# Optimization experiments

Measured on AMD Instinct MI355X. Metric: run time of the kernel, lower is better.

The kernel has to match this reference:

```python
import jax, jax.numpy as jnp
import numpy as np

B, S, D_IN = 4, 256, 1024
ATTN, HD = 1024, 64
H = ATTN // HD  # 16
C = 4096          # n_classes
R, CR, SC = 256, 1024, 2048  # n_roots, n_classroots, n_subclasses
FF = int(ATTN * 3.0)  # 3072
EPS = 1e-5


def setup_inputs() -> dict:
    key = jax.random.key(0)
    ks = jax.random.split(key, 16)
    x = jax.random.normal(ks[0], (B, S, D_IN), dtype=jnp.float32)
    cls = jax.random.normal(ks[1], (H, C, HD), dtype=jnp.float32)
    roots = jax.random.normal(ks[2], (H, R, HD), dtype=jnp.float32)
    # IndexedAdd indices: row 0 selects from src, row 1 scatters into dst
    clsroots_idx = jnp.stack([
        jax.random.randint(ks[3], (CR,), 0, R, dtype=jnp.int32),
        jax.random.randint(ks[4], (CR,), 0, C, dtype=jnp.int32)])
    clscls_idx = jnp.stack([
        jax.random.randint(ks[5], (SC,), 0, C, dtype=jnp.int32),
        jax.random.randint(ks[6], (SC,), 0, C, dtype=jnp.int32)])
    clsroots_w = jax.random.uniform(ks[7], (H, CR, 1), dtype=jnp.float32, minval=0.5, maxval=1.5)
    clscls_w = jax.random.uniform(ks[8], (H, SC, 1), dtype=jnp.float32, minval=0.5, maxval=1.5)
    sc = 1.0 / np.sqrt(D_IN)
    kv_w = jax.random.uniform(ks[9], (2 * ATTN, D_IN), dtype=jnp.float32, minval=-sc, maxval=sc)
    ln_gamma = jnp.ones((ATTN,), dtype=jnp.float32)
    ln_beta = jnp.zeros((ATTN,), dtype=jnp.float32)
    sa = 1.0 / np.sqrt(ATTN)
    ff_in_w = jax.random.uniform(ks[10], (2 * FF, ATTN), dtype=jnp.float32, minval=-sa, maxval=sa)
    sf = 1.0 / np.sqrt(FF)
    ff_out_w = jax.random.uniform(ks[11], (ATTN, FF), dtype=jnp.float32, minval=-sf, maxval=sf)
    out_w = jax.random.uniform(ks[12], (C, ATTN, 2), dtype=jnp.float32, minval=-sa, maxval=sa)
    return {"x": x, "cls": cls, "roots": roots, "clsroots_w": clsroots_w,
            "clscls_w": clscls_w, "kv_w": kv_w, "ln_gamma": ln_gamma, "ln_beta": ln_beta,
            "ff_in_w": ff_in_w, "ff_out_w": ff_out_w, "out_w": out_w,
            "clsroots_idx": clsroots_idx, "clscls_idx": clscls_idx}


def _rmsnorm(t):
    return t * jax.lax.rsqrt(jnp.mean(t * t, axis=-1, keepdims=True) + EPS)


def _silu(t):
    return t * jax.nn.sigmoid(t)


def reference(x, cls, roots, clsroots_w, clscls_w, kv_w, ln_gamma, ln_beta,
              ff_in_w, ff_out_w, out_w, clsroots_idx, clscls_idx):
    # --- hierarchical query build (IndexedAdd chain) ---
    qr = _rmsnorm(roots)                                        # [H,R,E]
    q = cls.at[:, clsroots_idx[1], :].add(qr[:, clsroots_idx[0], :] * clsroots_w)
    q_det = jax.lax.stop_gradient(q)                            # clscls uses q.detach()
    q = q.at[:, clscls_idx[1], :].add(q_det[:, clscls_idx[0], :] * clscls_w)
    q = _rmsnorm(q)                                             # [H,C,E]
    # --- KV projection + QK-RMSNorm cross-attention ---
    kv = (x @ kv_w.T).reshape(B, S, 2, H, HD)                   # '(n h e)' split
    k = jnp.transpose(kv[:, :, 0], (0, 2, 1, 3))                # [B,H,S,E]
    v = jnp.transpose(kv[:, :, 1], (0, 2, 1, 3))                # [B,H,S,E]
    k = _rmsnorm(k)
    scores = jnp.einsum('hce,bhse->bhcs', q, k) / np.sqrt(HD)   # [B,H,C,S]
    attn = jax.nn.softmax(scores, axis=-1)
    o = jnp.einsum('bhcs,bhse->bhce', attn, v)                  # [B,H,C,E]
    o = jnp.transpose(o, (0, 2, 1, 3)).reshape(B, C, ATTN)      # [B,C,ATTN]
    # --- SwiGLU FFN with pre-LayerNorm + residual ---
    mu = jnp.mean(o, axis=-1, keepdims=True)
    var = jnp.mean((o - mu) ** 2, axis=-1, keepdims=True)
    f = (o - mu) * jax.lax.rsqrt(var + EPS) * ln_gamma + ln_beta
    f = f @ ff_in_w.T                                           # [B,C,2*FF]
    f1, f2 = f[..., :FF], f[..., FF:]
    h = (_silu(f1) * f2) @ ff_out_w.T
    z = o + h                                                   # [B,C,ATTN]
    # --- per-class BatchLinear + SwiGLU output ---
    y = jnp.einsum('bca,cao->bco', z, out_w)                    # [B,C,2]
    out = _silu(y[..., 0:1]) * y[..., 1:2]                      # [B,C,1]
    return out
```

## Files before the change

kernel.cpp:

```cpp
#include <hip/hip_runtime.h>
#include <math.h>

#define EPS 1e-5f

typedef __bf16 bf16x8 __attribute__((ext_vector_type(8)));
typedef __bf16 bf16x4 __attribute__((ext_vector_type(4)));
typedef float f32x4 __attribute__((ext_vector_type(4)));

#define GPTR(p) ((const __attribute__((address_space(1))) void*)(p))
#define LPTR(p) ((__attribute__((address_space(3))) void*)(p))

__device__ __forceinline__ float wave_sum(float v) {
#pragma unroll
    for (int o = 32; o; o >>= 1) v += __shfl_xor(v, o);
    return v;
}

__global__ __launch_bounds__(256) void scatter1(const float* __restrict__ roots,
                                                const float* __restrict__ w,
                                                const int* __restrict__ idx,
                                                float* __restrict__ q) {
    int unit = (blockIdx.x << 2) + (threadIdx.x >> 6);
    int lane = threadIdx.x & 63;
    int h = unit >> 10;
    int i = unit & 1023;
    int r = idx[i];
    int c = idx[1024 + i];
    float val = roots[(h * 256 + r) * 64 + lane];
    float ss = wave_sum(val * val);
    float rs = rsqrtf(ss * (1.f / 64.f) + EPS);
    atomicAdd(&q[(h * 4096 + c) * 64 + lane], val * rs * w[(h << 10) + i]);
}

__global__ __launch_bounds__(256) void scatter2(const float* __restrict__ qdet,
                                                const float* __restrict__ w,
                                                const int* __restrict__ idx,
                                                float* __restrict__ q) {
    int unit = (blockIdx.x << 2) + (threadIdx.x >> 6);
    int lane = threadIdx.x & 63;
    int h = unit >> 11;
    int i = unit & 2047;
    int c1 = idx[i];
    int c2 = idx[2048 + i];
    float val = qdet[(h * 4096 + c1) * 64 + lane] * w[(h << 11) + i];
    atomicAdd(&q[(h * 4096 + c2) * 64 + lane], val);
}

__global__ __launch_bounds__(256) void rms_q_bf(const float* __restrict__ q,
                                                __bf16* __restrict__ qb) {
    int unit = (blockIdx.x << 2) + (threadIdx.x >> 6);
    int lane = threadIdx.x & 63;
    float v = q[(size_t)unit * 64 + lane];
    float ss = wave_sum(v * v);
    float r = v * rsqrtf(ss * (1.f / 64.f) + EPS);
    qb[(size_t)unit * 64 + lane] = (__bf16)r;
}

__global__ __launch_bounds__(256) void split8(const float* __restrict__ in,
                                              __bf16* __restrict__ hi,
                                              __bf16* __restrict__ lo, int n8) {
    int i = blockIdx.x * 256 + threadIdx.x;
    if (i >= n8) return;
    const float4* p = (const float4*)in + (size_t)i * 2;
    float4 u0 = p[0], u1 = p[1];
    float f[8] = {u0.x, u0.y, u0.z, u0.w, u1.x, u1.y, u1.z, u1.w};
    bf16x8 vh, vl;
#pragma unroll
    for (int j = 0; j < 8; ++j) {
        vh[j] = (__bf16)f[j];
        vl[j] = (__bf16)(f[j] - (float)vh[j]);
    }
    *((bf16x8*)hi + i) = vh;
    *((bf16x8*)lo + i) = vl;
}

__global__ __launch_bounds__(256) void gemm_kv_mfma(const __bf16* __restrict__ Ah,
                                                    const __bf16* __restrict__ Al,
                                                    const __bf16* __restrict__ Bh,
                                                    const __bf16* __restrict__ Bl,
                                                    float* __restrict__ Cout) {
    __shared__ __bf16 sAh[64 * 64], sAl[64 * 64];
    __shared__ __bf16 sBh[128 * 64], sBl[128 * 64];
    int tid = threadIdx.x;
    int bn = blockIdx.x, bm = blockIdx.y;
    int lane = tid & 63;
    int w = tid >> 6;
    int wr = (w >> 1) * 32, wc = (w & 1) * 64;
    int frow = lane & 15, fk = (lane >> 4) * 8;
    f32x4 acc[2][4] = {};
    const __bf16* Ahb = Ah + (size_t)(bm * 64) * 1024;
    const __bf16* Alb = Al + (size_t)(bm * 64) * 1024;
    const __bf16* Bhb = Bh + (size_t)(bn * 128) * 1024;
    const __bf16* Blb = Bl + (size_t)(bn * 128) * 1024;
    for (int k0 = 0; k0 < 1024; k0 += 64) {
#pragma unroll
        for (int t = 0; t < 2; ++t) {
            int e = (t * 256 + tid) * 8;
            int r = e >> 6, c = e & 63;
            __builtin_amdgcn_global_load_lds(GPTR(Ahb + (size_t)r * 1024 + k0 + c), LPTR(sAh + e), 16, 0, 0);
            __builtin_amdgcn_global_load_lds(GPTR(Alb + (size_t)r * 1024 + k0 + c), LPTR(sAl + e), 16, 0, 0);
        }
#pragma unroll
        for (int t = 0; t < 4; ++t) {
            int e = (t * 256 + tid) * 8;
            int r = e >> 6, c = e & 63;
            __builtin_amdgcn_global_load_lds(GPTR(Bhb + (size_t)r * 1024 + k0 + c), LPTR(sBh + e), 16, 0, 0);
            __builtin_amdgcn_global_load_lds(GPTR(Blb + (size_t)r * 1024 + k0 + c), LPTR(sBl + e), 16, 0, 0);
        }
        __syncthreads();
#pragma unroll
        for (int ks = 0; ks < 2; ++ks) {
            bf16x8 ah[2], al[2], bh2[4], bl2[4];
#pragma unroll
            for (int m = 0; m < 2; ++m) {
                ah[m] = *(const bf16x8*)(sAh + (wr + m * 16 + frow) * 64 + ks * 32 + fk);
                al[m] = *(const bf16x8*)(sAl + (wr + m * 16 + frow) * 64 + ks * 32 + fk);
            }
#pragma unroll
            for (int n = 0; n < 4; ++n) {
                bh2[n] = *(const bf16x8*)(sBh + (wc + n * 16 + frow) * 64 + ks * 32 + fk);
                bl2[n] = *(const bf16x8*)(sBl + (wc + n * 16 + frow) * 64 + ks * 32 + fk);
            }
#pragma unroll
            for (int m = 0; m < 2; ++m)
#pragma unroll
                for (int n = 0; n < 4; ++n) {
                    acc[m][n] = __builtin_amdgcn_mfma_f32_16x16x32_bf16(ah[m], bh2[n], acc[m][n], 0, 0, 0);
                    acc[m][n] = __builtin_amdgcn_mfma_f32_16x16x32_bf16(ah[m], bl2[n], acc[m][n], 0, 0, 0);
                    acc[m][n] = __builtin_amdgcn_mfma_f32_16x16x32_bf16(al[m], bh2[n], acc[m][n], 0, 0, 0);
                }
        }
        __syncthreads();
    }
    int crow = (lane >> 4) * 4, ccol = lane & 15;
#pragma unroll
    for (int m = 0; m < 2; ++m)
#pragma unroll
        for (int n = 0; n < 4; ++n)
#pragma unroll
            for (int j = 0; j < 4; ++j) {
                int row = bm * 64 + wr + m * 16 + crow + j;
                int col = bn * 128 + wc + n * 16 + ccol;
                Cout[(size_t)row * 2048 + col] = acc[m][n][j];
            }
}

__global__ __launch_bounds__(256) void kvsplit_bf(const float* __restrict__ kv,
                                                  __bf16* __restrict__ kb) {
    int unit = (blockIdx.x << 2) + (threadIdx.x >> 6);
    int lane = threadIdx.x & 63;
    int b = unit >> 12;
    int h = (unit >> 8) & 15;
    int s = unit & 255;
    float kvl = kv[(size_t)(b * 256 + s) * 2048 + (h << 6) + lane];
    float ss = wave_sum(kvl * kvl);
    float kn = kvl * rsqrtf(ss * (1.f / 64.f) + EPS);
    kb[(size_t)unit * 64 + lane] = (__bf16)kn;
}

__global__ __launch_bounds__(256) void vtrans_bf(const float* __restrict__ kv,
                                                 __bf16* __restrict__ vt) {
    __shared__ float T[64][65];
    int bh = blockIdx.x >> 2;
    int sc = blockIdx.x & 3;
    int b = bh >> 4, h = bh & 15;
    int tid = threadIdx.x;
    int s0 = sc * 64;
    int sl = tid >> 2, d0 = (tid & 3) * 16;
    const float* src = kv + (size_t)(b * 256 + s0 + sl) * 2048 + 1024 + (h << 6) + d0;
#pragma unroll
    for (int t = 0; t < 4; ++t) {
        float4 v4 = *(const float4*)(src + t * 4);
        T[sl][d0 + t * 4 + 0] = v4.x;
        T[sl][d0 + t * 4 + 1] = v4.y;
        T[sl][d0 + t * 4 + 2] = v4.z;
        T[sl][d0 + t * 4 + 3] = v4.w;
    }
    __syncthreads();
    int dr = tid >> 2, c0 = (tid & 3) * 16;
    bf16x8 h0, h1;
#pragma unroll
    for (int jj = 0; jj < 8; ++jj) h0[jj] = (__bf16)T[c0 + jj][dr];
#pragma unroll
    for (int jj = 0; jj < 8; ++jj) h1[jj] = (__bf16)T[c0 + 8 + jj][dr];
    size_t base = (size_t)bh * 16384 + (size_t)dr * 256 + s0 + c0;
    *(bf16x8*)(vt + base) = h0;
    *(bf16x8*)(vt + base + 8) = h1;
}

__global__ __launch_bounds__(256) void attn_mfma(const __bf16* __restrict__ qb,
                                                 const __bf16* __restrict__ kb,
                                                 const __bf16* __restrict__ vtb,
                                                 __bf16* __restrict__ ob) {
    __shared__ __bf16 P[64 * 264];
    __shared__ float wred[8][64];
    __shared__ float denomL[64];
    __shared__ __bf16 Ot[64 * 72];

    int wg = blockIdx.x;
    int swz = (wg & 7) * 512 + (wg >> 3);
    int bh = swz >> 6;
    int qt = swz & 63;
    int b = bh >> 4, h = bh & 15;
    int tid = threadIdx.x;
    int lane = tid & 63;
    int w = tid >> 6;
    int frow = lane & 15;
    int fk = (lane >> 4) * 8;
    int crow = (lane >> 4) * 4;
    int ccol = lane & 15;
    int q0 = qt * 64;
    int wsr = w * 64;

    const __bf16* kh = kb + (size_t)bh * 16384;
    const __bf16* qh = qb + (size_t)h * 262144 + (size_t)q0 * 64;

    f32x4 acc[4][4] = {};
#pragma unroll
    for (int ks = 0; ks < 2; ++ks) {
        bf16x8 kf[4];
#pragma unroll
        for (int m = 0; m < 4; ++m)
            kf[m] = *(const bf16x8*)(kh + (wsr + m * 16 + frow) * 64 + ks * 32 + fk);
#pragma unroll
        for (int n = 0; n < 4; ++n) {
            bf16x8 qf = *(const bf16x8*)(qh + (n * 16 + frow) * 64 + ks * 32 + fk);
#pragma unroll
            for (int m = 0; m < 4; ++m)
                acc[m][n] = __builtin_amdgcn_mfma_f32_16x16x32_bf16(kf[m], qf, acc[m][n], 0, 0, 0);
        }
    }
#pragma unroll
    for (int m = 0; m < 4; ++m)
#pragma unroll
        for (int n = 0; n < 4; ++n)
#pragma unroll
            for (int j = 0; j < 4; ++j) acc[m][n][j] *= 0.125f;

    float lm[4];
#pragma unroll
    for (int n = 0; n < 4; ++n) {
        float v = -1e30f;
#pragma unroll
        for (int m = 0; m < 4; ++m)
#pragma unroll
            for (int j = 0; j < 4; ++j) v = fmaxf(v, acc[m][n][j]);
        v = fmaxf(v, __shfl_xor(v, 16));
        v = fmaxf(v, __shfl_xor(v, 32));
        lm[n] = v;
    }
    if (lane < 16) {
#pragma unroll
        for (int n = 0; n < 4; ++n) wred[w][n * 16 + lane] = lm[n];
    }
    __syncthreads();
    float gm[4];
#pragma unroll
    for (int n = 0; n < 4; ++n) {
        int qq = n * 16 + ccol;
        gm[n] = fmaxf(fmaxf(wred[0][qq], wred[1][qq]), fmaxf(wred[2][qq], wred[3][qq]));
    }
    float lsum[4] = {0.f, 0.f, 0.f, 0.f};
#pragma unroll
    for (int m = 0; m < 4; ++m)
#pragma unroll
        for (int n = 0; n < 4; ++n)
#pragma unroll
            for (int j = 0; j < 4; ++j) {
                float p = __expf(acc[m][n][j] - gm[n]);
                acc[m][n][j] = p;
                lsum[n] += p;
            }
#pragma unroll
    for (int n = 0; n < 4; ++n) {
        float v = lsum[n];
        v += __shfl_xor(v, 16);
        v += __shfl_xor(v, 32);
        lsum[n] = v;
    }
    if (lane < 16) {
#pragma unroll
        for (int n = 0; n < 4; ++n) wred[4 + w][n * 16 + lane] = lsum[n];
    }
#pragma unroll
    for (int m = 0; m < 4; ++m)
#pragma unroll
        for (int n = 0; n < 4; ++n) {
            bf16x4 pv;
#pragma unroll
            for (int j = 0; j < 4; ++j) pv[j] = (__bf16)acc[m][n][j];
            *(bf16x4*)(P + (n * 16 + ccol) * 264 + wsr + m * 16 + crow) = pv;
        }
    __syncthreads();
    if (tid < 64)
        denomL[tid] = wred[4][tid] + wred[5][tid] + wred[6][tid] + wred[7][tid];

    const __bf16* vh = vtb + (size_t)bh * 16384;
    f32x4 accO[4] = {};
#pragma unroll
    for (int ks = 0; ks < 8; ++ks) {
        bf16x8 pf = *(const bf16x8*)(P + (w * 16 + frow) * 264 + ks * 32 + fk);
#pragma unroll
        for (int m = 0; m < 4; ++m) {
            bf16x8 vf = *(const bf16x8*)(vh + (m * 16 + frow) * 256 + ks * 32 + fk);
            accO[m] = __builtin_amdgcn_mfma_f32_16x16x32_bf16(vf, pf, accO[m], 0, 0, 0);
        }
    }
    __syncthreads();
    float rd = 1.0f / denomL[w * 16 + ccol];
#pragma unroll
    for (int m = 0; m < 4; ++m) {
        bf16x4 ov;
#pragma unroll
        for (int j = 0; j < 4; ++j) ov[j] = (__bf16)(accO[m][j] * rd);
        *(bf16x4*)(Ot + (w * 16 + ccol) * 72 + m * 16 + crow) = ov;
    }
    __syncthreads();
    {
        int qq = tid >> 2, dc = tid & 3;
        bf16x8 o0 = *(const bf16x8*)(Ot + qq * 72 + dc * 16);
        bf16x8 o1 = *(const bf16x8*)(Ot + qq * 72 + dc * 16 + 8);
        size_t base = (size_t)((b << 12) + q0 + qq) * 1024 + (h << 6) + dc * 16;
        *(bf16x8*)(ob + base) = o0;
        *(bf16x8*)(ob + base + 8) = o1;
    }
}

__global__ __launch_bounds__(256) void cvt_bf16(const float* __restrict__ in,
                                                __bf16* __restrict__ out, int n8) {
    int i = blockIdx.x * 256 + threadIdx.x;
    if (i >= n8) return;
    const float4* p = (const float4*)in + (size_t)i * 2;
    float4 u0 = p[0], u1 = p[1];
    bf16x8 v;
    v[0] = (__bf16)u0.x; v[1] = (__bf16)u0.y; v[2] = (__bf16)u0.z; v[3] = (__bf16)u0.w;
    v[4] = (__bf16)u1.x; v[5] = (__bf16)u1.y; v[6] = (__bf16)u1.z; v[7] = (__bf16)u1.w;
    *((bf16x8*)out + i) = v;
}

__global__ __launch_bounds__(256) void ln_stats(const __bf16* __restrict__ ob,
                                                float* __restrict__ mu,
                                                float* __restrict__ rstd) {
    __shared__ float r0[4], r1[4];
    int row = blockIdx.x;
    int tid = threadIdx.x;
    const bf16x4* op = (const bf16x4*)(ob + (size_t)row * 1024);
    bf16x4 v = op[tid];
    float s = 0, sq = 0;
#pragma unroll
    for (int j = 0; j < 4; ++j) { float f = (float)v[j]; s += f; sq += f * f; }
    s = wave_sum(s);
    sq = wave_sum(sq);
    if ((tid & 63) == 0) { r0[tid >> 6] = s; r1[tid >> 6] = sq; }
    __syncthreads();
    if (tid == 0) {
        float S = r0[0] + r0[1] + r0[2] + r0[3];
        float Q = r1[0] + r1[1] + r1[2] + r1[3];
        float m = S * (1.f / 1024.f);
        float var = Q * (1.f / 1024.f) - m * m;
        mu[row] = m;
        rstd[row] = rsqrtf(var + EPS);
    }
}

__global__ __launch_bounds__(256) void ln_apply(const __bf16* __restrict__ ob,
                                                const float* __restrict__ mu,
                                                const float* __restrict__ rstd,
                                                const float* __restrict__ gamma,
                                                const float* __restrict__ beta,
                                                __bf16* __restrict__ f, int R0) {
    int i = blockIdx.x * 256 + threadIdx.x;
    int row = i >> 7;
    int c8 = (i & 127) * 8;
    int gr = R0 + row;
    float m = mu[gr], rs = rstd[gr];
    bf16x8 ov = *((const bf16x8*)(ob + (size_t)gr * 1024 + c8));
    bf16x8 r;
#pragma unroll
    for (int j = 0; j < 8; ++j) {
        float v = (float)ov[j];
        r[j] = (__bf16)((v - m) * rs * gamma[c8 + j] + beta[c8 + j]);
    }
    *((bf16x8*)(f + (size_t)row * 1024 + c8)) = r;
}

__global__ __launch_bounds__(256) void gemm1_mfma(const __bf16* __restrict__ A,
                                                  const __bf16* __restrict__ W,
                                                  __bf16* __restrict__ U) {
    __shared__ __bf16 sA[128 * 64];
    __shared__ __bf16 sB1[128 * 64];
    __shared__ __bf16 sB2[128 * 64];
    const int K = 1024;
    int tid = threadIdx.x;
    int bn = blockIdx.x, bm = blockIdx.y;
    int lane = tid & 63;
    int w = tid >> 6;
    int wr = (w >> 1) * 64, wc = (w & 1) * 64;
    f32x4 acc1[4][4] = {};
    f32x4 acc2[4][4] = {};
    const __bf16* Ab = A + (size_t)(bm * 128) * K;
    const __bf16* B1b = W + (size_t)(bn * 128) * K;
    const __bf16* B2b = W + (size_t)(3072 + bn * 128) * K;
    int frow = lane & 15, fk = (lane >> 4) * 8;
    for (int k0 = 0; k0 < K; k0 += 64) {
#pragma unroll
        for (int t = 0; t < 4; ++t) {
            int e = (t * 256 + tid) * 8;
            int r = e >> 6, c = e & 63;
            __builtin_amdgcn_global_load_lds(GPTR(Ab + (size_t)r * K + k0 + c), LPTR(sA + e), 16, 0, 0);
            __builtin_amdgcn_global_load_lds(GPTR(B1b + (size_t)r * K + k0 + c), LPTR(sB1 + e), 16, 0, 0);
            __builtin_amdgcn_global_load_lds(GPTR(B2b + (size_t)r * K + k0 + c), LPTR(sB2 + e), 16, 0, 0);
        }
        __syncthreads();
#pragma unroll
        for (int ks = 0; ks < 2; ++ks) {
            bf16x8 a[4], b1[4], b2[4];
#pragma unroll
            for (int m = 0; m < 4; ++m)
                a[m] = *(const bf16x8*)(sA + (wr + m * 16 + frow) * 64 + ks * 32 + fk);
#pragma unroll
            for (int n = 0; n < 4; ++n) {
                b1[n] = *(const bf16x8*)(sB1 + (wc + n * 16 + frow) * 64 + ks * 32 + fk);
                b2[n] = *(const bf16x8*)(sB2 + (wc + n * 16 + frow) * 64 + ks * 32 + fk);
            }
#pragma unroll
            for (int m = 0; m < 4; ++m)
#pragma unroll
                for (int n = 0; n < 4; ++n) {
                    acc1[m][n] = __builtin_amdgcn_mfma_f32_16x16x32_bf16(a[m], b1[n], acc1[m][n], 0, 0, 0);
                    acc2[m][n] = __builtin_amdgcn_mfma_f32_16x16x32_bf16(a[m], b2[n], acc2[m][n], 0, 0, 0);
                }
        }
        __syncthreads();
    }
    int crow = (lane >> 4) * 4, ccol = lane & 15;
#pragma unroll
    for (int m = 0; m < 4; ++m)
#pragma unroll
        for (int n = 0; n < 4; ++n)
#pragma unroll
            for (int j = 0; j < 4; ++j) {
                float f1 = acc1[m][n][j], f2 = acc2[m][n][j];
                float sg = f1 / (1.f + expf(-f1));
                int row = bm * 128 + wr + m * 16 + crow + j;
                int col = bn * 128 + wc + n * 16 + ccol;
                U[(size_t)row * 3072 + col] = (__bf16)(sg * f2);
            }
}

__global__ __launch_bounds__(256) void gemm2_mfma(const __bf16* __restrict__ U,
                                                  const __bf16* __restrict__ W2,
                                                  __bf16* __restrict__ Oz) {
    __shared__ __bf16 sA[128 * 64];
    __shared__ __bf16 sB[128 * 64];
    const int K = 3072;
    int tid = threadIdx.x;
    int bn = blockIdx.x, bm = blockIdx.y;
    int lane = tid & 63;
    int w = tid >> 6;
    int wr = (w >> 1) * 64, wc = (w & 1) * 64;
    f32x4 acc[4][4] = {};
    const __bf16* Ab = U + (size_t)(bm * 128) * K;
    const __bf16* Bb = W2 + (size_t)(bn * 128) * K;
    int frow = lane & 15, fk = (lane >> 4) * 8;
    for (int k0 = 0; k0 < K; k0 += 64) {
#pragma unroll
        for (int t = 0; t < 4; ++t) {
            int e = (t * 256 + tid) * 8;
            int r = e >> 6, c = e & 63;
            __builtin_amdgcn_global_load_lds(GPTR(Ab + (size_t)r * K + k0 + c), LPTR(sA + e), 16, 0, 0);
            __builtin_amdgcn_global_load_lds(GPTR(Bb + (size_t)r * K + k0 + c), LPTR(sB + e), 16, 0, 0);
        }
        __syncthreads();
#pragma unroll
        for (int ks = 0; ks < 2; ++ks) {
            bf16x8 a[4], b[4];
#pragma unroll
            for (int m = 0; m < 4; ++m)
                a[m] = *(const bf16x8*)(sA + (wr + m * 16 + frow) * 64 + ks * 32 + fk);
#pragma unroll
            for (int n = 0; n < 4; ++n)
                b[n] = *(const bf16x8*)(sB + (wc + n * 16 + frow) * 64 + ks * 32 + fk);
#pragma unroll
            for (int m = 0; m < 4; ++m)
#pragma unroll
                for (int n = 0; n < 4; ++n)
                    acc[m][n] = __builtin_amdgcn_mfma_f32_16x16x32_bf16(a[m], b[n], acc[m][n], 0, 0, 0);
        }
        __syncthreads();
    }
    int crow = (lane >> 4) * 4, ccol = lane & 15;
#pragma unroll
    for (int m = 0; m < 4; ++m)
#pragma unroll
        for (int n = 0; n < 4; ++n)
#pragma unroll
            for (int j = 0; j < 4; ++j) {
                int row = bm * 128 + wr + m * 16 + crow + j;
                int col = bn * 128 + wc + n * 16 + ccol;
                size_t off = (size_t)row * 1024 + col;
                float z = (float)Oz[off] + acc[m][n][j];
                Oz[off] = (__bf16)z;
            }
}

__global__ __launch_bounds__(256) void out_proj4(const __bf16* __restrict__ z,
                                                 const float* __restrict__ ow,
                                                 float* __restrict__ out) {
    __shared__ float red[4][8];
    int c = blockIdx.x;
    int tid = threadIdx.x;
    int a0 = tid * 4;
    const float4* w4 = (const float4*)(ow + (size_t)c * 2048);
    float4 wA = w4[tid * 2];
    float4 wB = w4[tid * 2 + 1];
    float y[8];
#pragma unroll
    for (int jj = 0; jj < 8; ++jj) y[jj] = 0.f;
#pragma unroll
    for (int bb = 0; bb < 4; ++bb) {
        bf16x4 zv = *(const bf16x4*)(z + (size_t)((bb << 12) + c) * 1024 + a0);
        float z0 = (float)zv[0], z1 = (float)zv[1], z2 = (float)zv[2], z3 = (float)zv[3];
        y[2 * bb] += z0 * wA.x + z1 * wA.z + z2 * wB.x + z3 * wB.z;
        y[2 * bb + 1] += z0 * wA.y + z1 * wA.w + z2 * wB.y + z3 * wB.w;
    }
#pragma unroll
    for (int jj = 0; jj < 8; ++jj) y[jj] = wave_sum(y[jj]);
    if ((tid & 63) == 0) {
#pragma unroll
        for (int jj = 0; jj < 8; ++jj) red[tid >> 6][jj] = y[jj];
    }
    __syncthreads();
    if (tid < 4) {
        float a0s = red[0][2 * tid] + red[1][2 * tid] + red[2][2 * tid] + red[3][2 * tid];
        float a1s = red[0][2 * tid + 1] + red[1][2 * tid + 1] + red[2][2 * tid + 1] + red[3][2 * tid + 1];
        out[(size_t)tid * 4096 + c] = a0s / (1.f + expf(-a0s)) * a1s;
    }
}

extern "C" void kernel_launch(void* const* d_in, const int* in_sizes, int n_in,
                              void* d_out, int out_size, void* d_ws, size_t ws_size,
                              hipStream_t stream) {
    const float* x = (const float*)d_in[0];
    const float* cls = (const float*)d_in[1];
    const float* roots = (const float*)d_in[2];
    const float* crw = (const float*)d_in[3];
    const float* ccw = (const float*)d_in[4];
    const float* kv_w = (const float*)d_in[5];
    const float* gamma = (const float*)d_in[6];
    const float* beta = (const float*)d_in[7];
    const float* ffin = (const float*)d_in[8];
    const float* ffout = (const float*)d_in[9];
    const float* ow = (const float*)d_in[10];
    const int* cridx = (const int*)d_in[11];
    const int* ccidx = (const int*)d_in[12];
    float* out = (float*)d_out;

    float* ws = (float*)d_ws;
    float* q = ws;
    float* kvb = ws + 4194304;
    __bf16* kbf = (__bf16*)(ws + 6291456);
    __bf16* vtb = (__bf16*)(ws + 6815744);
    __bf16* o_bf = (__bf16*)(ws + 8388608);
    __bf16* xhi = (__bf16*)(ws + 8388608);
    __bf16* xlo = (__bf16*)(ws + 8912896);
    __bf16* kvwhi = (__bf16*)(ws + 9437184);
    __bf16* kvwlo = (__bf16*)(ws + 10485760);
    float* qdet = ws + 16777216;
    __bf16* qbf = (__bf16*)(ws + 20971520);
    __bf16* w1bf = (__bf16*)ws;
    __bf16* w2bf = (__bf16*)(ws + 3145728);
    float* mu = ws + 4718592;
    float* rstd = mu + 16384;
    __bf16* fbf = (__bf16*)(ws + 16777216);
    __bf16* u_s = (__bf16*)(ws + 18874368);

    hipMemcpyAsync(q, cls, 4194304 * sizeof(float), hipMemcpyDeviceToDevice, stream);
    scatter1<<<4096, 256, 0, stream>>>(roots, crw, cridx, q);
    hipMemcpyAsync(qdet, q, 4194304 * sizeof(float), hipMemcpyDeviceToDevice, stream);
    scatter2<<<8192, 256, 0, stream>>>(qdet, ccw, ccidx, q);
    rms_q_bf<<<16384, 256, 0, stream>>>(q, qbf);
    split8<<<512, 256, 0, stream>>>(x, xhi, xlo, 131072);
    split8<<<1024, 256, 0, stream>>>(kv_w, kvwhi, kvwlo, 262144);
    gemm_kv_mfma<<<dim3(16, 16), 256, 0, stream>>>(xhi, xlo, kvwhi, kvwlo, kvb);
    kvsplit_bf<<<4096, 256, 0, stream>>>(kvb, kbf);
    vtrans_bf<<<256, 256, 0, stream>>>(kvb, vtb);
    attn_mfma<<<4096, 256, 0, stream>>>(qbf, kbf, vtb, o_bf);

    cvt_bf16<<<3072, 256, 0, stream>>>(ffin, w1bf, 786432);
    cvt_bf16<<<1536, 256, 0, stream>>>(ffout, w2bf, 393216);
    ln_stats<<<16384, 256, 0, stream>>>(o_bf, mu, rstd);
    for (int sl = 0; sl < 4; ++sl) {
        int R0 = sl * 4096;
        ln_apply<<<2048, 256, 0, stream>>>(o_bf, mu, rstd, gamma, beta, fbf, R0);
        gemm1_mfma<<<dim3(24, 32), 256, 0, stream>>>(fbf, w1bf, u_s);
        gemm2_mfma<<<dim3(8, 32), 256, 0, stream>>>(u_s, w2bf, o_bf + (size_t)R0 * 1024);
    }
    out_proj4<<<4096, 256, 0, stream>>>(o_bf, ow, out);
}
```

Baseline: 1.023 ms.

## Halve gemm1 accumulators via LDS exchange and shrink gemm2 M-tile

gemm1 now computes a 128x64 tile of both gate and up projections in a single accumulator set: half the waves compute the gate columns, the other half the up columns, and the gate results are exchanged through reused shared memory before the SiLU-multiply epilogue. This halves accumulator registers and shared memory per block and doubles the grid, aiming for higher occupancy and better CU fill. gemm2 tiles shrink from 128x128 to 64x128, doubling its block count. The trade-off is an extra LDS round trip and barrier in gemm1, half the waves idle during its epilogue, and lower per-block arithmetic intensity in both kernels.

```diff
diff --git a/kernel.cpp b/kernel.cpp
--- a/kernel.cpp
+++ b/kernel.cpp
@@ -387,20 +387,20 @@
 __global__ __launch_bounds__(256) void gemm1_mfma(const __bf16* __restrict__ A,
                                                   const __bf16* __restrict__ W,
                                                   __bf16* __restrict__ U) {
-    __shared__ __bf16 sA[128 * 64];
-    __shared__ __bf16 sB1[128 * 64];
-    __shared__ __bf16 sB2[128 * 64];
+    __shared__ __align__(16) unsigned char smemraw[32768];
+    __bf16* sA = (__bf16*)smemraw;
+    __bf16* sB = (__bf16*)(smemraw + 16384);
+    float* sEx = (float*)smemraw;
     const int K = 1024;
     int tid = threadIdx.x;
     int bn = blockIdx.x, bm = blockIdx.y;
     int lane = tid & 63;
     int w = tid >> 6;
     int wr = (w >> 1) * 64, wc = (w & 1) * 64;
-    f32x4 acc1[4][4] = {};
-    f32x4 acc2[4][4] = {};
+    f32x4 acc[4][4] = {};
     const __bf16* Ab = A + (size_t)(bm * 128) * K;
-    const __bf16* B1b = W + (size_t)(bn * 128) * K;
-    const __bf16* B2b = W + (size_t)(3072 + bn * 128) * K;
+    const __bf16* B1b = W + (size_t)(bn * 64) * K;
+    const __bf16* B2b = W + (size_t)(3072 + bn * 64) * K;
     int frow = lane & 15, fk = (lane >> 4) * 8;
     for (int k0 = 0; k0 < K; k0 += 64) {
 #pragma unroll
@@ -408,81 +408,105 @@
             int e = (t * 256 + tid) * 8;
             int r = e >> 6, c = e & 63;
             __builtin_amdgcn_global_load_lds(GPTR(Ab + (size_t)r * K + k0 + c), LPTR(sA + e), 16, 0, 0);
-            __builtin_amdgcn_global_load_lds(GPTR(B1b + (size_t)r * K + k0 + c), LPTR(sB1 + e), 16, 0, 0);
-            __builtin_amdgcn_global_load_lds(GPTR(B2b + (size_t)r * K + k0 + c), LPTR(sB2 + e), 16, 0, 0);
+        }
+#pragma unroll
+        for (int t = 0; t < 2; ++t) {
+            int e = (t * 256 + tid) * 8;
+            int r = e >> 6, c = e & 63;
+            __builtin_amdgcn_global_load_lds(GPTR(B1b + (size_t)r * K + k0 + c), LPTR(sB + e), 16, 0, 0);
+        }
+#pragma unroll
+        for (int t = 2; t < 4; ++t) {
+            int e = (t * 256 + tid) * 8;
+            int r = (e >> 6) - 64, c = e & 63;
+            __builtin_amdgcn_global_load_lds(GPTR(B2b + (size_t)r * K + k0 + c), LPTR(sB + e), 16, 0, 0);
         }
         __syncthreads();
 #pragma unroll
         for (int ks = 0; ks < 2; ++ks) {
-            bf16x8 a[4], b1[4], b2[4];
+            bf16x8 a[4], b[4];
 #pragma unroll
             for (int m = 0; m < 4; ++m)
                 a[m] = *(const bf16x8*)(sA + (wr + m * 16 + frow) * 64 + ks * 32 + fk);
 #pragma unroll
-            for (int n = 0; n < 4; ++n) {
-                b1[n] = *(const bf16x8*)(sB1 + (wc + n * 16 + frow) * 64 + ks * 32 + fk);
-                b2[n] = *(const bf16x8*)(sB2 + (wc + n * 16 + frow) * 64 + ks * 32 + fk);
-            }
+            for (int n = 0; n < 4; ++n)
+                b[n] = *(const bf16x8*)(sB + (wc + n * 16 + frow) * 64 + ks * 32 + fk);
 #pragma unroll
             for (int m = 0; m < 4; ++m)
 #pragma unroll
-                for (int n = 0; n < 4; ++n) {
-                    acc1[m][n] = __builtin_amdgcn_mfma_f32_16x16x32_bf16(a[m], b1[n], acc1[m][n], 0, 0, 0);
-                    acc2[m][n] = __builtin_amdgcn_mfma_f32_16x16x32_bf16(a[m], b2[n], acc2[m][n], 0, 0, 0);
+                for (int n = 0; n < 4; ++n)
+                    acc[m][n] = __builtin_amdgcn_mfma_f32_16x16x32_bf16(a[m], b[n], acc[m][n], 0, 0, 0);
+        }
+        __syncthreads();
+    }
+    int crow = (lane >> 4) * 4, ccol = lane & 15;
+    if ((w & 1) == 0) {
+#pragma unroll
+        for (int m = 0; m < 4; ++m)
+#pragma unroll
+            for (int n = 0; n < 4; ++n)
+#pragma unroll
+                for (int j = 0; j < 4; ++j)
+                    sEx[(wr + m * 16 + crow + j) * 64 + n * 16 + ccol] = acc[m][n][j];
+    }
+    __syncthreads();
+    if (w & 1) {
+#pragma unroll
+        for (int m = 0; m < 4; ++m)
+#pragma unroll
+            for (int n = 0; n < 4; ++n)
+#pragma unroll
+                for (int j = 0; j < 4; ++j) {
+                    int row = wr + m * 16 + crow + j;
+                    int col = n * 16 + ccol;
+                    float f1 = sEx[row * 64 + col];
+                    float f2 = acc[m][n][j];
+                    float sg = f1 / (1.f + expf(-f1));
+                    U[(size_t)(bm * 128 + row) * 3072 + bn * 64 + col] = (__bf16)(sg * f2);
                 }
-        }
-        __syncthreads();
-    }
-    int crow = (lane >> 4) * 4, ccol = lane & 15;
-#pragma unroll
-    for (int m = 0; m < 4; ++m)
-#pragma unroll
-        for (int n = 0; n < 4; ++n)
-#pragma unroll
-            for (int j = 0; j < 4; ++j) {
-                float f1 = acc1[m][n][j], f2 = acc2[m][n][j];
-                float sg = f1 / (1.f + expf(-f1));
-                int row = bm * 128 + wr + m * 16 + crow + j;
-                int col = bn * 128 + wc + n * 16 + ccol;
-                U[(size_t)row * 3072 + col] = (__bf16)(sg * f2);
-            }
+    }
 }
 
 __global__ __launch_bounds__(256) void gemm2_mfma(const __bf16* __restrict__ U,
                                                   const __bf16* __restrict__ W2,
                                                   __bf16* __restrict__ Oz) {
-    __shared__ __bf16 sA[128 * 64];
+    __shared__ __bf16 sA[64 * 64];
     __shared__ __bf16 sB[128 * 64];
     const int K = 3072;
     int tid = threadIdx.x;
     int bn = blockIdx.x, bm = blockIdx.y;
     int lane = tid & 63;
     int w = tid >> 6;
-    int wr = (w >> 1) * 64, wc = (w & 1) * 64;
-    f32x4 acc[4][4] = {};
-    const __bf16* Ab = U + (size_t)(bm * 128) * K;
+    int wr = (w >> 1) * 32, wc = (w & 1) * 64;
+    f32x4 acc[2][4] = {};
+    const __bf16* Ab = U + (size_t)(bm * 64) * K;
     const __bf16* Bb = W2 + (size_t)(bn * 128) * K;
     int frow = lane & 15, fk = (lane >> 4) * 8;
     for (int k0 = 0; k0 < K; k0 += 64) {
 #pragma unroll
+        for (int t = 0; t < 2; ++t) {
+            int e = (t * 256 + tid) * 8;
+            int r = e >> 6, c = e & 63;
+            __builtin_amdgcn_global_load_lds(GPTR(Ab + (size_t)r * K + k0 + c), LPTR(sA + e), 16, 0, 0);
+        }
+#pragma unroll
         for (int t = 0; t < 4; ++t) {
             int e = (t * 256 + tid) * 8;
             int r = e >> 6, c = e & 63;
-            __builtin_amdgcn_global_load_lds(GPTR(Ab + (size_t)r * K + k0 + c), LPTR(sA + e), 16, 0, 0);
             __builtin_amdgcn_global_load_lds(GPTR(Bb + (size_t)r * K + k0 + c), LPTR(sB + e), 16, 0, 0);
         }
         __syncthreads();
 #pragma unroll
         for (int ks = 0; ks < 2; ++ks) {
-            bf16x8 a[4], b[4];
-#pragma unroll
-            for (int m = 0; m < 4; ++m)
+            bf16x8 a[2], b[4];
+#pragma unroll
+            for (int m = 0; m < 2; ++m)
                 a[m] = *(const bf16x8*)(sA + (wr + m * 16 + frow) * 64 + ks * 32 + fk);
 #pragma unroll
             for (int n = 0; n < 4; ++n)
                 b[n] = *(const bf16x8*)(sB + (wc + n * 16 + frow) * 64 + ks * 32 + fk);
 #pragma unroll
-            for (int m = 0; m < 4; ++m)
+            for (int m = 0; m < 2; ++m)
 #pragma unroll
                 for (int n = 0; n < 4; ++n)
                     acc[m][n] = __builtin_amdgcn_mfma_f32_16x16x32_bf16(a[m], b[n], acc[m][n], 0, 0, 0);
@@ -491,12 +515,12 @@
     }
     int crow = (lane >> 4) * 4, ccol = lane & 15;
 #pragma unroll
-    for (int m = 0; m < 4; ++m)
+    for (int m = 0; m < 2; ++m)
 #pragma unroll
         for (int n = 0; n < 4; ++n)
 #pragma unroll
             for (int j = 0; j < 4; ++j) {
-                int row = bm * 128 + wr + m * 16 + crow + j;
+                int row = bm * 64 + wr + m * 16 + crow + j;
                 int col = bn * 128 + wc + n * 16 + ccol;
                 size_t off = (size_t)row * 1024 + col;
                 float z = (float)Oz[off] + acc[m][n][j];
@@ -593,8 +617,8 @@
     for (int sl = 0; sl < 4; ++sl) {
         int R0 = sl * 4096;
         ln_apply<<<2048, 256, 0, stream>>>(o_bf, mu, rstd, gamma, beta, fbf, R0);
-        gemm1_mfma<<<dim3(24, 32), 256, 0, stream>>>(fbf, w1bf, u_s);
-        gemm2_mfma<<<dim3(8, 32), 256, 0, stream>>>(u_s, w2bf, o_bf + (size_t)R0 * 1024);
+        gemm1_mfma<<<dim3(48, 32), 256, 0, stream>>>(fbf, w1bf, u_s);
+        gemm2_mfma<<<dim3(8, 64), 256, 0, stream>>>(u_s, w2bf, o_bf + (size_t)R0 * 1024);
     }
     out_proj4<<<4096, 256, 0, stream>>>(o_bf, ow, out);
 }
```

New measurement: 900.0 us. -12.0%, faster.
